# Optimization experiments

Measured on AMD Instinct MI355X. Metric: run time of the kernel, lower is better.

## Reference

```python
import jax, jax.numpy as jnp
import numpy as np

NUM_USERS = 100000
NUM_ITEMS = 50000
EMBED_DIM = 64
NUM_LAYERS = 3
NNZ = 4800000  # 2 * num_interactions (symmetric bipartite adjacency)


def setup_inputs() -> dict:
    key = jax.random.key(0)
    k_u, k_i, k_r, k_c, k_v = jax.random.split(key, 5)
    N = NUM_USERS + NUM_ITEMS
    E = NNZ // 2
    # Xavier-uniform-style embeddings (any float init is fine for a math reference)
    user_emb = jax.random.normal(k_u, (NUM_USERS, EMBED_DIM), dtype=jnp.float32) * 0.1
    item_emb = jax.random.normal(k_i, (NUM_ITEMS, EMBED_DIM), dtype=jnp.float32) * 0.1
    # Build a symmetric bipartite COO adjacency: user->item and item->user edges.
    u = jax.random.randint(k_r, (E,), 0, NUM_USERS, dtype=jnp.int32)
    i = jax.random.randint(k_c, (E,), NUM_USERS, N, dtype=jnp.int32)
    adj_rows = jnp.concatenate([u, i])
    adj_cols = jnp.concatenate([i, u])
    # Normalized adjacency values (D^-1/2 A D^-1/2 in real LightGCN); random positive here.
    v = jax.random.uniform(k_v, (E,), dtype=jnp.float32, minval=0.01, maxval=0.1)
    adj_vals = jnp.concatenate([v, v])
    return {"user_emb": user_emb, "item_emb": item_emb, "adj_vals": adj_vals,
            "adj_rows": adj_rows, "adj_cols": adj_cols}


def reference(user_emb, item_emb, adj_vals, adj_rows, adj_cols):
    num_users = user_emb.shape[0]
    N = num_users + item_emb.shape[0]
    ego = jnp.concatenate([user_emb, item_emb], axis=0)  # [N, D]
    x = ego
    acc = ego  # running sum across layers (fused layer-mean)
    for _ in range(NUM_LAYERS):
        # SpMM: gather source embeddings, scale by edge value, scatter-add to rows.
        x = jax.ops.segment_sum(adj_vals[:, None] * x[adj_cols], adj_rows,
                                num_segments=N)
        acc = acc + x
    final = acc / jnp.asarray(NUM_LAYERS + 1, dtype=ego.dtype)
    return final[:num_users], final[num_users:]
```

## Files before the change

### kernel.cpp

```cpp
#include <hip/hip_runtime.h>

static constexpr int NUSERS = 100000;
static constexpr int NITEMS = 50000;
static constexpr int NNODES = NUSERS + NITEMS;
static constexpr int D      = 64;
static constexpr int NNZE   = 4800000;
static constexpr int NVEC4  = NNODES * D / 4;
static constexpr int NU4    = NUSERS * D / 4;

static constexpr int NB       = 512;
static constexpr int RPB      = (NNODES + NB - 1) / NB;
static constexpr int CHUNK    = 8192;
static constexpr int P1_BLOCKS = (NNZE + CHUNK - 1) / CHUNK;

__device__ __forceinline__ unsigned bf16rne(float f) {
    unsigned u = __float_as_uint(f);
    return (u + 0x7FFFu + ((u >> 16) & 1u)) >> 16;
}
__device__ __forceinline__ float bflo(unsigned u) { return __uint_as_float(u << 16); }
__device__ __forceinline__ float bfhi(unsigned u) { return __uint_as_float(u & 0xFFFF0000u); }

__global__ void lg_init(const float4* __restrict__ ue, const float4* __restrict__ ie,
                        uint2* __restrict__ x, float4* __restrict__ out) {
    int stride = gridDim.x * blockDim.x;
    for (int i = blockIdx.x * blockDim.x + threadIdx.x; i < NVEC4; i += stride) {
        float4 v = (i < NU4) ? ue[i] : ie[i - NU4];
        out[i] = v;
        x[i] = make_uint2(bf16rne(v.x) | (bf16rne(v.y) << 16),
                          bf16rne(v.z) | (bf16rne(v.w) << 16));
    }
}

__global__ void __launch_bounds__(256)
lg_bcnt(const int* __restrict__ rows, int* __restrict__ bucketCnt) {
    __shared__ int cnt[NB];
    int tid = threadIdx.x;
    for (int b = tid; b < NB; b += 256) cnt[b] = 0;
    __syncthreads();
    int c0 = blockIdx.x * CHUNK;
    int c1 = min(c0 + CHUNK, NNZE);
    for (int e = c0 + tid; e < c1; e += 256)
        atomicAdd(&cnt[rows[e] / RPB], 1);
    __syncthreads();
    for (int b = tid; b < NB; b += 256)
        if (cnt[b]) atomicAdd(&bucketCnt[b], cnt[b]);
}

__global__ void __launch_bounds__(512)
lg_bscan(const int* __restrict__ bucketCnt, int* __restrict__ bbase,
         int* __restrict__ gcur) {
    __shared__ int s[NB];
    int t = threadIdx.x;
    int v = bucketCnt[t];
    s[t] = v;
    __syncthreads();
    for (int off = 1; off < NB; off <<= 1) {
        int tmp = (t >= off) ? s[t - off] : 0;
        __syncthreads();
        s[t] += tmp;
        __syncthreads();
    }
    int ex = s[t] - v;
    bbase[t] = ex;
    gcur[t] = ex;
    if (t == NB - 1) bbase[NB] = s[t];
}

__global__ void __launch_bounds__(256)
lg_part1(const int* __restrict__ rows, const int* __restrict__ cols,
         const float* __restrict__ vals, int* __restrict__ gcur,
         int2* __restrict__ stage) {
    __shared__ int cnt[NB];
    __shared__ int base[NB];
    int tid = threadIdx.x;
    int c0 = blockIdx.x * CHUNK;
    int c1 = min(c0 + CHUNK, NNZE);
    for (int b = tid; b < NB; b += 256) cnt[b] = 0;
    __syncthreads();
    for (int e = c0 + tid; e < c1; e += 256)
        atomicAdd(&cnt[rows[e] / RPB], 1);
    __syncthreads();
    for (int b = tid; b < NB; b += 256) {
        int n = cnt[b];
        base[b] = n ? atomicAdd(&gcur[b], n) : 0;
        cnt[b] = 0;
    }
    __syncthreads();
    for (int e = c0 + tid; e < c1; e += 256) {
        int r = rows[e];
        int b = r / RPB;
        int rl = r - b * RPB;
        int k = atomicAdd(&cnt[b], 1);
        stage[base[b] + k] = make_int2(cols[e] | (rl << 18), __float_as_int(vals[e]));
    }
}

__global__ void __launch_bounds__(512)
lg_part2(const int* __restrict__ bbase, const int2* __restrict__ stage,
         int2* __restrict__ csr, int* __restrict__ rowptr) {
    __shared__ int s[NB];
    __shared__ int lcur[RPB];
    int b = blockIdx.x;
    int t = threadIdx.x;
    int r0 = b * RPB;
    int nrows = min(RPB, NNODES - r0);
    int s0 = bbase[b], s1 = bbase[b + 1];

    s[t] = 0;
    __syncthreads();
    for (int p = s0 + t; p < s1; p += 512)
        atomicAdd(&s[(stage[p].x >> 18) & 511], 1);
    __syncthreads();
    int v = s[t];
    for (int off = 1; off < NB; off <<= 1) {
        int tmp = (t >= off) ? s[t - off] : 0;
        __syncthreads();
        s[t] += tmp;
        __syncthreads();
    }
    int pos0 = s0 + s[t] - v;
    if (t < nrows) {
        rowptr[r0 + t] = pos0;
        lcur[t] = pos0;
    }
    if (b == gridDim.x - 1 && t == 0) rowptr[NNODES] = NNZE;
    __syncthreads();
    for (int p = s0 + t; p < s1; p += 512) {
        int2 cv = stage[p];
        int rl = (cv.x >> 18) & 511;
        int pos = atomicAdd(&lcur[rl], 1);
        csr[pos] = make_int2(cv.x & 0x3FFFF, cv.y);
    }
}

template<int MODE>
__global__ void __launch_bounds__(256)
lg_spmm(const int* __restrict__ rowptr, const int2* __restrict__ csr,
        const uint2* __restrict__ x, uint2* __restrict__ y, float4* __restrict__ out) {
    int lane16 = threadIdx.x & 15;
    int r = (blockIdx.x * blockDim.x + threadIdx.x) >> 4;
    if (r >= NNODES) return;
    int p0 = rowptr[r], p1 = rowptr[r + 1];
    float4 acc = {0.f, 0.f, 0.f, 0.f};
    int p = p0;
    for (; p + 4 <= p1; p += 4) {
        int2 cv0 = csr[p], cv1 = csr[p + 1], cv2 = csr[p + 2], cv3 = csr[p + 3];
        uint2 x0 = x[cv0.x * 16 + lane16];
        uint2 x1 = x[cv1.x * 16 + lane16];
        uint2 x2 = x[cv2.x * 16 + lane16];
        uint2 x3 = x[cv3.x * 16 + lane16];
        float v0 = __int_as_float(cv0.y), v1 = __int_as_float(cv1.y);
        float v2 = __int_as_float(cv2.y), v3 = __int_as_float(cv3.y);
        acc.x += v0 * bflo(x0.x) + v1 * bflo(x1.x) + v2 * bflo(x2.x) + v3 * bflo(x3.x);
        acc.y += v0 * bfhi(x0.x) + v1 * bfhi(x1.x) + v2 * bfhi(x2.x) + v3 * bfhi(x3.x);
        acc.z += v0 * bflo(x0.y) + v1 * bflo(x1.y) + v2 * bflo(x2.y) + v3 * bflo(x3.y);
        acc.w += v0 * bfhi(x0.y) + v1 * bfhi(x1.y) + v2 * bfhi(x2.y) + v3 * bfhi(x3.y);
    }
    for (; p < p1; ++p) {
        int2 cv = csr[p];
        uint2 xv = x[cv.x * 16 + lane16];
        float v = __int_as_float(cv.y);
        acc.x += v * bflo(xv.x); acc.y += v * bfhi(xv.x);
        acc.z += v * bflo(xv.y); acc.w += v * bfhi(xv.y);
    }
    int idx = r * 16 + lane16;
    if (MODE == 0) {
        y[idx] = make_uint2(bf16rne(acc.x) | (bf16rne(acc.y) << 16),
                            bf16rne(acc.z) | (bf16rne(acc.w) << 16));
        float4 o = out[idx];
        o.x += acc.x; o.y += acc.y; o.z += acc.z; o.w += acc.w;
        out[idx] = o;
    } else {
        float4 o = out[idx];
        o.x = (o.x + acc.x) * 0.25f;
        o.y = (o.y + acc.y) * 0.25f;
        o.z = (o.z + acc.z) * 0.25f;
        o.w = (o.w + acc.w) * 0.25f;
        out[idx] = o;
    }
}

extern "C" void kernel_launch(void* const* d_in, const int* in_sizes, int n_in,
                              void* d_out, int out_size, void* d_ws, size_t ws_size,
                              hipStream_t stream) {
    const float* ue   = (const float*)d_in[0];
    const float* ie   = (const float*)d_in[1];
    const float* vals = (const float*)d_in[2];
    const int*   rows = (const int*)d_in[3];
    const int*   cols = (const int*)d_in[4];
    float* out = (float*)d_out;

    uint2* xa     = (uint2*)d_ws;
    uint2* xb     = xa + NVEC4;
    int2*  csr    = (int2*)(xb + NVEC4);
    int2*  stage  = csr + NNZE;
    int*   rowptr = (int*)(stage + NNZE);
    int*   bucketCnt = rowptr + (NNODES + 1);
    int*   bbase  = bucketCnt + NB;
    int*   gcur   = bbase + (NB + 1);

    const int BLK = 256;
    const int spmmBlocks = NNODES * 16 / BLK;

    lg_init<<<2048, BLK, 0, stream>>>((const float4*)ue, (const float4*)ie, xa, (float4*)out);
    hipMemsetAsync(bucketCnt, 0, NB * sizeof(int), stream);
    lg_bcnt<<<P1_BLOCKS, BLK, 0, stream>>>(rows, bucketCnt);
    lg_bscan<<<1, NB, 0, stream>>>(bucketCnt, bbase, gcur);
    lg_part1<<<P1_BLOCKS, BLK, 0, stream>>>(rows, cols, vals, gcur, stage);
    lg_part2<<<NB, 512, 0, stream>>>(bbase, stage, csr, rowptr);

    lg_spmm<0><<<spmmBlocks, BLK, 0, stream>>>(rowptr, csr, xa, xb, (float4*)out);
    lg_spmm<0><<<spmmBlocks, BLK, 0, stream>>>(rowptr, csr, xb, xa, (float4*)out);
    lg_spmm<1><<<spmmBlocks, BLK, 0, stream>>>(rowptr, csr, xa, nullptr, (float4*)out);
}
```

Baseline: 391.0 us.

## Stage partition writes through LDS and defer layer accumulation to a combine kernel

```diff
diff --git a/kernel.cpp b/kernel.cpp
--- a/kernel.cpp
+++ b/kernel.cpp
@@ -10,7 +10,7 @@
 
 static constexpr int NB       = 512;
 static constexpr int RPB      = (NNODES + NB - 1) / NB;
-static constexpr int CHUNK    = 8192;
+static constexpr int CHUNK    = 4096;
 static constexpr int P1_BLOCKS = (NNZE + CHUNK - 1) / CHUNK;
 
 __device__ __forceinline__ unsigned bf16rne(float f) {
@@ -21,29 +21,37 @@
 __device__ __forceinline__ float bfhi(unsigned u) { return __uint_as_float(u & 0xFFFF0000u); }
 
 __global__ void lg_init(const float4* __restrict__ ue, const float4* __restrict__ ie,
-                        uint2* __restrict__ x, float4* __restrict__ out) {
+                        uint2* __restrict__ x) {
     int stride = gridDim.x * blockDim.x;
     for (int i = blockIdx.x * blockDim.x + threadIdx.x; i < NVEC4; i += stride) {
         float4 v = (i < NU4) ? ue[i] : ie[i - NU4];
-        out[i] = v;
         x[i] = make_uint2(bf16rne(v.x) | (bf16rne(v.y) << 16),
                           bf16rne(v.z) | (bf16rne(v.w) << 16));
     }
 }
 
-__global__ void __launch_bounds__(256)
+__global__ void __launch_bounds__(512)
 lg_bcnt(const int* __restrict__ rows, int* __restrict__ bucketCnt) {
     __shared__ int cnt[NB];
-    int tid = threadIdx.x;
-    for (int b = tid; b < NB; b += 256) cnt[b] = 0;
+    int t = threadIdx.x;
+    cnt[t] = 0;
     __syncthreads();
     int c0 = blockIdx.x * CHUNK;
     int c1 = min(c0 + CHUNK, NNZE);
-    for (int e = c0 + tid; e < c1; e += 256)
-        atomicAdd(&cnt[rows[e] / RPB], 1);
-    __syncthreads();
-    for (int b = tid; b < NB; b += 256)
-        if (cnt[b]) atomicAdd(&bucketCnt[b], cnt[b]);
+    #pragma unroll
+    for (int pass = 0; pass < 2; ++pass) {
+        int e = c0 + (pass * 512 + t) * 4;
+        if (e < c1) {
+            int4 r4 = *(const int4*)(rows + e);
+            atomicAdd(&cnt[r4.x / RPB], 1);
+            atomicAdd(&cnt[r4.y / RPB], 1);
+            atomicAdd(&cnt[r4.z / RPB], 1);
+            atomicAdd(&cnt[r4.w / RPB], 1);
+        }
+    }
+    __syncthreads();
+    int n = cnt[t];
+    if (n) atomicAdd(&bucketCnt[t], n);
 }
 
 __global__ void __launch_bounds__(512)
@@ -66,32 +74,88 @@
     if (t == NB - 1) bbase[NB] = s[t];
 }
 
-__global__ void __launch_bounds__(256)
+__global__ void __launch_bounds__(512)
 lg_part1(const int* __restrict__ rows, const int* __restrict__ cols,
          const float* __restrict__ vals, int* __restrict__ gcur,
          int2* __restrict__ stage) {
-    __shared__ int cnt[NB];
-    __shared__ int base[NB];
-    int tid = threadIdx.x;
+    __shared__ int s_cnt[NB];
+    __shared__ int s_lcur[NB];
+    __shared__ int s_gofs[NB];
+    __shared__ int2 s_pay[CHUNK];
+    __shared__ unsigned short s_bid[CHUNK];
+    int t = threadIdx.x;
     int c0 = blockIdx.x * CHUNK;
     int c1 = min(c0 + CHUNK, NNZE);
-    for (int b = tid; b < NB; b += 256) cnt[b] = 0;
-    __syncthreads();
-    for (int e = c0 + tid; e < c1; e += 256)
-        atomicAdd(&cnt[rows[e] / RPB], 1);
-    __syncthreads();
-    for (int b = tid; b < NB; b += 256) {
-        int n = cnt[b];
-        base[b] = n ? atomicAdd(&gcur[b], n) : 0;
-        cnt[b] = 0;
-    }
-    __syncthreads();
-    for (int e = c0 + tid; e < c1; e += 256) {
-        int r = rows[e];
-        int b = r / RPB;
-        int rl = r - b * RPB;
-        int k = atomicAdd(&cnt[b], 1);
-        stage[base[b] + k] = make_int2(cols[e] | (rl << 18), __float_as_int(vals[e]));
+    s_cnt[t] = 0;
+    __syncthreads();
+
+    int  eb[8], ep[8]; float ev[8];
+    bool has0, has1;
+    {
+        int e = c0 + t * 4;
+        has0 = e < c1;
+        if (has0) {
+            int4 r4 = *(const int4*)(rows + e);
+            int4 c4 = *(const int4*)(cols + e);
+            float4 v4 = *(const float4*)(vals + e);
+            eb[0] = r4.x / RPB; ep[0] = c4.x | ((r4.x - eb[0] * RPB) << 18); ev[0] = v4.x;
+            eb[1] = r4.y / RPB; ep[1] = c4.y | ((r4.y - eb[1] * RPB) << 18); ev[1] = v4.y;
+            eb[2] = r4.z / RPB; ep[2] = c4.z | ((r4.z - eb[2] * RPB) << 18); ev[2] = v4.z;
+            eb[3] = r4.w / RPB; ep[3] = c4.w | ((r4.w - eb[3] * RPB) << 18); ev[3] = v4.w;
+            atomicAdd(&s_cnt[eb[0]], 1); atomicAdd(&s_cnt[eb[1]], 1);
+            atomicAdd(&s_cnt[eb[2]], 1); atomicAdd(&s_cnt[eb[3]], 1);
+        }
+        e = c0 + (512 + t) * 4;
+        has1 = e < c1;
+        if (has1) {
+            int4 r4 = *(const int4*)(rows + e);
+            int4 c4 = *(const int4*)(cols + e);
+            float4 v4 = *(const float4*)(vals + e);
+            eb[4] = r4.x / RPB; ep[4] = c4.x | ((r4.x - eb[4] * RPB) << 18); ev[4] = v4.x;
+            eb[5] = r4.y / RPB; ep[5] = c4.y | ((r4.y - eb[5] * RPB) << 18); ev[5] = v4.y;
+            eb[6] = r4.z / RPB; ep[6] = c4.z | ((r4.z - eb[6] * RPB) << 18); ev[6] = v4.z;
+            eb[7] = r4.w / RPB; ep[7] = c4.w | ((r4.w - eb[7] * RPB) << 18); ev[7] = v4.w;
+            atomicAdd(&s_cnt[eb[4]], 1); atomicAdd(&s_cnt[eb[5]], 1);
+            atomicAdd(&s_cnt[eb[6]], 1); atomicAdd(&s_cnt[eb[7]], 1);
+        }
+    }
+    __syncthreads();
+
+    int myCnt = s_cnt[t];
+    for (int off = 1; off < NB; off <<= 1) {
+        int tmp = (t >= off) ? s_cnt[t - off] : 0;
+        __syncthreads();
+        s_cnt[t] += tmp;
+        __syncthreads();
+    }
+    int lstart = s_cnt[t] - myCnt;
+    int gbase = myCnt ? atomicAdd(&gcur[t], myCnt) : 0;
+    s_lcur[t] = lstart;
+    s_gofs[t] = gbase - lstart;
+    __syncthreads();
+
+    #pragma unroll
+    for (int k = 0; k < 4; ++k) {
+        if (has0) {
+            int pos = atomicAdd(&s_lcur[eb[k]], 1);
+            s_pay[pos] = make_int2(ep[k], __float_as_int(ev[k]));
+            s_bid[pos] = (unsigned short)eb[k];
+        }
+    }
+    #pragma unroll
+    for (int k = 4; k < 8; ++k) {
+        if (has1) {
+            int pos = atomicAdd(&s_lcur[eb[k]], 1);
+            s_pay[pos] = make_int2(ep[k], __float_as_int(ev[k]));
+            s_bid[pos] = (unsigned short)eb[k];
+        }
+    }
+    __syncthreads();
+
+    int n = c1 - c0;
+    for (int p = t; p < n; p += 512) {
+        int b = s_bid[p];
+        stage[s_gofs[b] + p] = s_pay[p];
     }
 }
 
@@ -133,10 +197,9 @@
     }
 }
 
-template<int MODE>
 __global__ void __launch_bounds__(256)
 lg_spmm(const int* __restrict__ rowptr, const int2* __restrict__ csr,
-        const uint2* __restrict__ x, uint2* __restrict__ y, float4* __restrict__ out) {
+        const uint2* __restrict__ x, uint2* __restrict__ y) {
     int lane16 = threadIdx.x & 15;
     int r = (blockIdx.x * blockDim.x + threadIdx.x) >> 4;
     if (r >= NNODES) return;
@@ -163,20 +226,23 @@
         acc.x += v * bflo(xv.x); acc.y += v * bfhi(xv.x);
         acc.z += v * bflo(xv.y); acc.w += v * bfhi(xv.y);
     }
-    int idx = r * 16 + lane16;
-    if (MODE == 0) {
-        y[idx] = make_uint2(bf16rne(acc.x) | (bf16rne(acc.y) << 16),
-                            bf16rne(acc.z) | (bf16rne(acc.w) << 16));
-        float4 o = out[idx];
-        o.x += acc.x; o.y += acc.y; o.z += acc.z; o.w += acc.w;
-        out[idx] = o;
-    } else {
-        float4 o = out[idx];
-        o.x = (o.x + acc.x) * 0.25f;
-        o.y = (o.y + acc.y) * 0.25f;
-        o.z = (o.z + acc.z) * 0.25f;
-        o.w = (o.w + acc.w) * 0.25f;
-        out[idx] = o;
+    y[r * 16 + lane16] = make_uint2(bf16rne(acc.x) | (bf16rne(acc.y) << 16),
+                                    bf16rne(acc.z) | (bf16rne(acc.w) << 16));
+}
+
+__global__ void lg_combine(const float4* __restrict__ ue, const float4* __restrict__ ie,
+                           const uint2* __restrict__ y1, const uint2* __restrict__ y2,
+                           const uint2* __restrict__ y3, float4* __restrict__ out) {
+    int stride = gridDim.x * blockDim.x;
+    for (int i = blockIdx.x * blockDim.x + threadIdx.x; i < NVEC4; i += stride) {
+        float4 e = (i < NU4) ? ue[i] : ie[i - NU4];
+        uint2 a = y1[i], b = y2[i], c = y3[i];
+        float4 o;
+        o.x = (e.x + bflo(a.x) + bflo(b.x) + bflo(c.x)) * 0.25f;
+        o.y = (e.y + bfhi(a.x) + bfhi(b.x) + bfhi(c.x)) * 0.25f;
+        o.z = (e.z + bflo(a.y) + bflo(b.y) + bflo(c.y)) * 0.25f;
+        o.w = (e.w + bfhi(a.y) + bfhi(b.y) + bfhi(c.y)) * 0.25f;
+        out[i] = o;
     }
 }
 
@@ -194,22 +260,25 @@
     uint2* xb     = xa + NVEC4;
     int2*  csr    = (int2*)(xb + NVEC4);
     int2*  stage  = csr + NNZE;
+    uint2* y3     = (uint2*)stage;
     int*   rowptr = (int*)(stage + NNZE);
     int*   bucketCnt = rowptr + (NNODES + 1);
     int*   bbase  = bucketCnt + NB;
     int*   gcur   = bbase + (NB + 1);
 
-    const int BLK = 256;
-    const int spmmBlocks = NNODES * 16 / BLK;
-
-    lg_init<<<2048, BLK, 0, stream>>>((const float4*)ue, (const float4*)ie, xa, (float4*)out);
+    const int spmmBlocks = NNODES * 16 / 256;
+
+    lg_init<<<2048, 256, 0, stream>>>((const float4*)ue, (const float4*)ie, xa);
     hipMemsetAsync(bucketCnt, 0, NB * sizeof(int), stream);
-    lg_bcnt<<<P1_BLOCKS, BLK, 0, stream>>>(rows, bucketCnt);
+    lg_bcnt<<<P1_BLOCKS, 512, 0, stream>>>(rows, bucketCnt);
     lg_bscan<<<1, NB, 0, stream>>>(bucketCnt, bbase, gcur);
-    lg_part1<<<P1_BLOCKS, BLK, 0, stream>>>(rows, cols, vals, gcur, stage);
+    lg_part1<<<P1_BLOCKS, 512, 0, stream>>>(rows, cols, vals, gcur, stage);
     lg_part2<<<NB, 512, 0, stream>>>(bbase, stage, csr, rowptr);
 
-    lg_spmm<0><<<spmmBlocks, BLK, 0, stream>>>(rowptr, csr, xa, xb, (float4*)out);
-    lg_spmm<0><<<spmmBlocks, BLK, 0, stream>>>(rowptr, csr, xb, xa, (float4*)out);
-    lg_spmm<1><<<spmmBlocks, BLK, 0, stream>>>(rowptr, csr, xa, nullptr, (float4*)out);
-}
+    lg_spmm<<<spmmBlocks, 256, 0, stream>>>(rowptr, csr, xa, xb);
+    lg_spmm<<<spmmBlocks, 256, 0, stream>>>(rowptr, csr, xb, xa);
+    lg_spmm<<<spmmBlocks, 256, 0, stream>>>(rowptr, csr, xa, y3);
+
+    lg_combine<<<2048, 256, 0, stream>>>((const float4*)ue, (const float4*)ie,
+                                         xb, xa, y3, (float4*)out);
+}
```

New measurement: 373.5 us. -4.5%, faster.
